# Performance work log

Measured on AMD Instinct MI355X. Metric: run time of the kernel, lower is better.

The kernel has to match this reference:

```python
import jax, jax.numpy as jnp
import numpy as np

B, OBS, H, A, E = 131072, 194, 64, 5, 3  # batch, obs dim, hidden, max_action_dim, n event types


def setup_inputs() -> dict:
    key = jax.random.key(0)
    ks = jax.random.split(key, 16)
    s = lambda k, shape, std=0.1: (jax.random.normal(k, shape, dtype=jnp.float32) * std)
    return {
        "x": jax.random.normal(ks[0], (B, OBS), dtype=jnp.float32),
        "action": jax.random.randint(ks[1], (B,), 0, A),
        "W1": s(ks[2], (OBS, H)), "b1": jnp.zeros((H,), jnp.float32),
        "W2": s(ks[3], (H, H)),   "b2": jnp.zeros((H,), jnp.float32),
        "Wh": s(ks[4], (E, H, A), 0.01), "bh": jnp.zeros((E, A), jnp.float32),
        "Wc1": s(ks[5], (OBS, H)), "bc1": jnp.zeros((H,), jnp.float32),
        "Wc2": s(ks[6], (H, H)),   "bc2": jnp.zeros((H,), jnp.float32),
        "Wc3": s(ks[7], (H, 1)),   "bc3": jnp.zeros((1,), jnp.float32),
    }


def reference(x, action, W1, b1, W2, b2, Wh, bh, Wc1, bc1, Wc2, bc2, Wc3, bc3):
    # shared trunk
    feat = jnp.tanh(jnp.tanh(x @ W1 + b1) @ W2 + b2)          # [B, H]
    # route each sample to one of E heads via argmax of first 3 obs dims
    ev = jnp.argmax(x[:, :E], axis=1)                          # [B] int
    all_logits = jnp.einsum('bh,eha->bea', feat, Wh) + bh      # [B, E, A]
    logits = jnp.take_along_axis(
        all_logits, jnp.broadcast_to(ev[:, None, None], (x.shape[0], 1, A)), axis=1
    )[:, 0]                                                    # [B, A]
    logp_all = jax.nn.log_softmax(logits, axis=-1)             # [B, A]
    logp = jnp.take_along_axis(logp_all, action[:, None], axis=1)[:, 0]  # [B]
    entropy = -jnp.sum(jnp.exp(logp_all) * logp_all, axis=-1)  # [B]
    # critic
    value = jnp.tanh(jnp.tanh(x @ Wc1 + bc1) @ Wc2 + bc2) @ Wc3 + bc3    # [B, 1]
    return action, logp, entropy, value
```

## Files before the change

### kernel.cpp

```cpp
#include <hip/hip_runtime.h>
#include <hip/hip_bf16.h>

constexpr int Bt    = 131072;
constexpr int OBS   = 194;
constexpr int NT    = 512;
constexpr int ITERS = 4;
constexpr int RS    = 72;
constexpr int LS    = 18;

constexpr int ROLE_S = 23552;

constexpr int L_W1f = 0;
constexpr int L_W2f = 28672;
constexpr int L_WHf = 45056;
constexpr int L_H   = 47104;
constexpr int L_AUX = 65536;
constexpr int L_TOT = 70144;

typedef short bf8   __attribute__((ext_vector_type(8)));
typedef float f32x4 __attribute__((ext_vector_type(4)));
typedef unsigned int u32;

__device__ __forceinline__ short f2bs(float f) {
    union { __hip_bfloat16 h; short s; } u;
    u.h = __float2bfloat16(f);
    return u.s;
}
__device__ __forceinline__ float bs2f(short s) {
    union { short s; __hip_bfloat16 h; } u;
    u.s = s;
    return __bfloat162float(u.h);
}
__device__ __forceinline__ u32 pk2(float a, float b) {
    union { __hip_bfloat162 h; u32 u; } r;
    r.h = __float22bfloat162_rn(float2{a, b});
    return r.u;
}
__device__ __forceinline__ float fast_tanh(float v) {
    v = fminf(fmaxf(v, -15.f), 15.f);
    float e = __expf(2.f * v);
    return (e - 1.f) * __builtin_amdgcn_rcpf(e + 1.f);
}
__device__ __forceinline__ void dma16(const void* g, void* s) {
    __builtin_amdgcn_global_load_lds(
        (const __attribute__((address_space(1))) u32*)g,
        (__attribute__((address_space(3))) u32*)s, 16, 0, 0);
}

__global__ void __launch_bounds__(256) prep(
    const float* __restrict__ W1, const float* __restrict__ b1,
    const float* __restrict__ W2, const float* __restrict__ Wh,
    const float* __restrict__ Wc1, const float* __restrict__ bc1,
    const float* __restrict__ Wc2, const float* __restrict__ Wc3,
    short* __restrict__ ws)
{
    const int gid = blockIdx.x * 256 + threadIdx.x;
    const int gsz = gridDim.x * 256;

    for (int i = gid; i < 14336; i += gsz) {
        int j = i & 7, l = (i >> 3) & 63, nt = (i >> 9) & 3, kb = i >> 11;
        int k = kb * 32 + ((l >> 4) << 3) + j;
        int n = nt * 16 + (l & 15);
        short v1 = 0, v2 = 0;
        if (k < OBS) {
            v1 = f2bs(W1[k * 64 + n]);
            v2 = f2bs(Wc1[k * 64 + n]);
        } else if (k == OBS) {
            v1 = f2bs(b1[n]);
            v2 = f2bs(bc1[n]);
        }
        ws[i]          = v1;
        ws[ROLE_S + i] = v2;
    }
    for (int i = gid; i < 8192; i += gsz) {
        int j = i & 7, l = (i >> 3) & 63, nt = (i >> 9) & 3, kb = i >> 11;
        int s = kb * 32 + ((l >> 4) << 3) + j;
        int kp = (s & 3) * 16 + (s >> 2);
        int n = nt * 16 + (l & 15);
        ws[14336 + i]          = f2bs(W2[kp * 64 + n]);
        ws[ROLE_S + 14336 + i] = f2bs(Wc2[kp * 64 + n]);
    }
    for (int i = gid; i < 1024; i += gsz) {
        int j = i & 7, l = (i >> 3) & 63, kb = i >> 9;
        int s = kb * 32 + ((l >> 4) << 3) + j;
        int kp = (s & 3) * 16 + (s >> 2);
        int cc = l & 15;
        float v;
        if (cc == 15) v = Wc3[kp];
        else { int e = cc / 5, a = cc - 5 * e; v = Wh[(e * 64 + kp) * 5 + a]; }
        short vs = f2bs(v);
        ws[22528 + i]          = vs;
        ws[ROLE_S + 22528 + i] = vs;
    }
}

__global__ void __launch_bounds__(NT, 4) fused_ac(
    const float* __restrict__ x, const int* __restrict__ act_in,
    const float* __restrict__ b2, const float* __restrict__ bc2,
    const float* __restrict__ bh, const float* __restrict__ bc3,
    const short* __restrict__ ws,
    float* __restrict__ out)
{
    __shared__ __align__(16) char smem[L_TOT];

    const int t    = threadIdx.x;
    const int w    = t >> 6;
    const int l    = t & 63;
    const int q    = l >> 4;
    const int c    = l & 15;
    const int b    = blockIdx.x;
    const int g    = b >> 4;
    const int role = (b >> 3) & 1;
    const int sub  = b & 7;
    const int base = g * 4096 + sub * 512;

    {
        const char* gsrc = ((const char*)ws) + (size_t)role * 47104;
        #pragma unroll
        for (int i = 0; i < 6; ++i) {
            int idx = i * NT + t;
            if (idx < 2944)
                dma16(gsrc + idx * 16, smem + idx * 16);
        }
    }

    const float* bL2 = role ? bc2 : b2;
    float b2v[4];
    #pragma unroll
    for (int nt = 0; nt < 4; ++nt) b2v[nt] = bL2[nt * 16 + c];
    float bhv = role ? bc3[0] : ((c < 15) ? bh[c] : 0.f);

    __syncthreads();

    const bf8* fL1 = reinterpret_cast<const bf8*>(smem + L_W1f);
    const bf8* fL2 = reinterpret_cast<const bf8*>(smem + L_W2f);
    const bf8* fWh = reinterpret_cast<const bf8*>(smem + L_WHf);
    short* hb = reinterpret_cast<short*>(smem + L_H + w * 2304);
    short* lw = reinterpret_cast<short*>(smem + L_AUX + w * 576);
    float* vb = reinterpret_cast<float*>(smem + L_AUX + w * 576);

    #pragma unroll 1
    for (int i = 0; i < ITERS; ++i) {
        const int gm = base + i * 128 + w * 16 + c;

        float2 raw[24]; float2 rt6 = float2{0.f, 0.f};
        {
            const float* xr = x + (size_t)gm * OBS;
            #pragma unroll
            for (int kb = 0; kb < 6; ++kb) {
                const float2* p = reinterpret_cast<const float2*>(xr + kb * 32 + q * 8);
                raw[kb * 4 + 0] = p[0]; raw[kb * 4 + 1] = p[1];
                raw[kb * 4 + 2] = p[2]; raw[kb * 4 + 3] = p[3];
            }
            if (q == 0) rt6 = *reinterpret_cast<const float2*>(xr + 192);
        }
        int act = 0;
        if (role == 0 && l < 16) act = act_in[gm];

        union AF { u32 u[4]; bf8 v; } af[7];
        #pragma unroll
        for (int kb = 0; kb < 6; ++kb) {
            af[kb].u[0] = pk2(raw[kb * 4 + 0].x, raw[kb * 4 + 0].y);
            af[kb].u[1] = pk2(raw[kb * 4 + 1].x, raw[kb * 4 + 1].y);
            af[kb].u[2] = pk2(raw[kb * 4 + 2].x, raw[kb * 4 + 2].y);
            af[kb].u[3] = pk2(raw[kb * 4 + 3].x, raw[kb * 4 + 3].y);
        }
        af[6].u[0] = 0; af[6].u[1] = 0; af[6].u[2] = 0; af[6].u[3] = 0;
        if (q == 0) {
            af[6].u[0] = pk2(rt6.x, rt6.y);
            af[6].u[1] = pk2(1.0f, 0.0f);
        }
        int ev = 0;
        {
            float bbest = raw[0].x;
            if (raw[0].y > bbest) { bbest = raw[0].y; ev = 1; }
            if (raw[1].x > bbest) { ev = 2; }
        }

        f32x4 acc[4];
        #pragma unroll
        for (int nt = 0; nt < 4; ++nt) acc[nt] = f32x4{0.f, 0.f, 0.f, 0.f};
        #pragma unroll
        for (int kb = 0; kb < 7; ++kb) {
            bf8 a = af[kb].v;
            #pragma unroll
            for (int nt = 0; nt < 4; ++nt)
                acc[nt] = __builtin_amdgcn_mfma_f32_16x16x32_bf16(a, fL1[(kb * 4 + nt) * 64 + l], acc[nt], 0, 0, 0);
        }
        #pragma unroll
        for (int r = 0; r < 4; ++r) {
            uint2 pa;
            pa.x = pk2(fast_tanh(acc[0][r]), fast_tanh(acc[1][r]));
            pa.y = pk2(fast_tanh(acc[2][r]), fast_tanh(acc[3][r]));
            *reinterpret_cast<uint2*>(&hb[(q * 4 + r) * RS + 4 * c]) = pa;
        }

        #pragma unroll
        for (int nt = 0; nt < 4; ++nt)
            acc[nt] = f32x4{b2v[nt], b2v[nt], b2v[nt], b2v[nt]};
        #pragma unroll
        for (int kb = 0; kb < 2; ++kb) {
            bf8 xa = *reinterpret_cast<const bf8*>(&hb[c * RS + kb * 32 + q * 8]);
            #pragma unroll
            for (int nt = 0; nt < 4; ++nt)
                acc[nt] = __builtin_amdgcn_mfma_f32_16x16x32_bf16(xa, fL2[(kb * 4 + nt) * 64 + l], acc[nt], 0, 0, 0);
        }
        #pragma unroll
        for (int r = 0; r < 4; ++r) {
            uint2 pa;
            pa.x = pk2(fast_tanh(acc[0][r]), fast_tanh(acc[1][r]));
            pa.y = pk2(fast_tanh(acc[2][r]), fast_tanh(acc[3][r]));
            *reinterpret_cast<uint2*>(&hb[(q * 4 + r) * RS + 4 * c]) = pa;
        }

        {
            f32x4 hd = f32x4{bhv, bhv, bhv, bhv};
            #pragma unroll
            for (int kb = 0; kb < 2; ++kb) {
                bf8 bw = fWh[kb * 64 + l];
                bf8 fa = *reinterpret_cast<const bf8*>(&hb[c * RS + kb * 32 + q * 8]);
                hd = __builtin_amdgcn_mfma_f32_16x16x32_bf16(fa, bw, hd, 0, 0, 0);
            }
            if (role == 0) {
                #pragma unroll
                for (int r = 0; r < 4; ++r)
                    lw[(q * 4 + r) * LS + c] = f2bs(hd[r]);
            } else if (c == 15) {
                #pragma unroll
                for (int r = 0; r < 4; ++r)
                    vb[q * 4 + r] = hd[r];
            }
        }

        if (role == 0) {
            if (l < 16) {
                float lg[5];
                #pragma unroll
                for (int a = 0; a < 5; ++a)
                    lg[a] = bs2f(lw[c * LS + ev * 5 + a]);
                float mx = lg[0];
                #pragma unroll
                for (int a = 1; a < 5; ++a) mx = fmaxf(mx, lg[a]);
                float se = 0.f;
                #pragma unroll
                for (int a = 0; a < 5; ++a) se += __expf(lg[a] - mx);
                float lse = __logf(se) + mx;
                float lsel = lg[0];
                #pragma unroll
                for (int a = 1; a < 5; ++a) lsel = (act == a) ? lg[a] : lsel;
                float ent = 0.f;
                #pragma unroll
                for (int a = 0; a < 5; ++a) { float lp = lg[a] - lse; ent -= __expf(lp) * lp; }

                out[gm]          = (float)act;
                out[Bt + gm]     = lsel - lse;
                out[2 * Bt + gm] = ent;
            }
        } else {
            if (l < 16)
                out[3 * Bt + gm] = vb[c];
        }
    }
}

extern "C" void kernel_launch(void* const* d_in, const int* in_sizes, int n_in,
                              void* d_out, int out_size, void* d_ws, size_t ws_size,
                              hipStream_t stream) {
    const float* x   = (const float*)d_in[0];
    const int*   act = (const int*)  d_in[1];
    const float* W1  = (const float*)d_in[2];
    const float* b1  = (const float*)d_in[3];
    const float* W2  = (const float*)d_in[4];
    const float* b2  = (const float*)d_in[5];
    const float* Wh  = (const float*)d_in[6];
    const float* bh  = (const float*)d_in[7];
    const float* Wc1 = (const float*)d_in[8];
    const float* bc1 = (const float*)d_in[9];
    const float* Wc2 = (const float*)d_in[10];
    const float* bc2 = (const float*)d_in[11];
    const float* Wc3 = (const float*)d_in[12];
    const float* bc3 = (const float*)d_in[13];
    float* out = (float*)d_out;
    short* ws  = (short*)d_ws;

    hipLaunchKernelGGL(prep, dim3(32), dim3(256), 0, stream,
                       W1, b1, W2, Wh, Wc1, bc1, Wc2, Wc3, ws);
    hipLaunchKernelGGL(fused_ac, dim3(512), dim3(NT), 0, stream,
                       x, act, b2, bc2, bh, bc3, ws, out);
}
```

Measured before the change: 183.2 us.

## Prefetch next x tile, vectorize weight prep, simplify tanh and entropy math

The main kernel now loads the next iteration's x rows into registers before computing the current one, so global latency overlaps with MFMA work. The head weight fragments are hoisted out of the loop. tanh drops the clamp and uses 1-2/(e+1), and entropy is computed in one pass from the softmax sums. The prep kernel now has each thread build and store a 16-byte fragment, launched on fewer blocks. Prefetching raises register pressure and may cut occupancy. Without the clamp, tanh now relies on how exp and rcp behave at infinity for large inputs.

```diff
diff --git a/kernel.cpp b/kernel.cpp
--- a/kernel.cpp
+++ b/kernel.cpp
@@ -37,9 +37,8 @@
     return r.u;
 }
 __device__ __forceinline__ float fast_tanh(float v) {
-    v = fminf(fmaxf(v, -15.f), 15.f);
     float e = __expf(2.f * v);
-    return (e - 1.f) * __builtin_amdgcn_rcpf(e + 1.f);
+    return fmaf(-2.f, __builtin_amdgcn_rcpf(e + 1.f), 1.f);
 }
 __device__ __forceinline__ void dma16(const void* g, void* s) {
     __builtin_amdgcn_global_load_lds(
@@ -55,42 +54,57 @@
     short* __restrict__ ws)
 {
     const int gid = blockIdx.x * 256 + threadIdx.x;
-    const int gsz = gridDim.x * 256;
-
-    for (int i = gid; i < 14336; i += gsz) {
-        int j = i & 7, l = (i >> 3) & 63, nt = (i >> 9) & 3, kb = i >> 11;
-        int k = kb * 32 + ((l >> 4) << 3) + j;
+
+    if (gid < 1792) {
+        int fi = gid;
+        int l = fi & 63, nt = (fi >> 6) & 3, kb = fi >> 8;
         int n = nt * 16 + (l & 15);
-        short v1 = 0, v2 = 0;
-        if (k < OBS) {
-            v1 = f2bs(W1[k * 64 + n]);
-            v2 = f2bs(Wc1[k * 64 + n]);
-        } else if (k == OBS) {
-            v1 = f2bs(b1[n]);
-            v2 = f2bs(bc1[n]);
-        }
-        ws[i]          = v1;
-        ws[ROLE_S + i] = v2;
-    }
-    for (int i = gid; i < 8192; i += gsz) {
-        int j = i & 7, l = (i >> 3) & 63, nt = (i >> 9) & 3, kb = i >> 11;
-        int s = kb * 32 + ((l >> 4) << 3) + j;
-        int kp = (s & 3) * 16 + (s >> 2);
+        union { bf8 v; short s[8]; } v1, v2;
+        #pragma unroll
+        for (int j = 0; j < 8; ++j) {
+            int k = kb * 32 + ((l >> 4) << 3) + j;
+            short a = 0, bvs = 0;
+            if (k < OBS) {
+                a   = f2bs(W1[k * 64 + n]);
+                bvs = f2bs(Wc1[k * 64 + n]);
+            } else if (k == OBS) {
+                a   = f2bs(b1[n]);
+                bvs = f2bs(bc1[n]);
+            }
+            v1.s[j] = a; v2.s[j] = bvs;
+        }
+        *reinterpret_cast<bf8*>(ws + fi * 8)          = v1.v;
+        *reinterpret_cast<bf8*>(ws + ROLE_S + fi * 8) = v2.v;
+    } else if (gid < 1792 + 1024) {
+        int fi = gid - 1792;
+        int l = fi & 63, nt = (fi >> 6) & 3, kb = fi >> 8;
         int n = nt * 16 + (l & 15);
-        ws[14336 + i]          = f2bs(W2[kp * 64 + n]);
-        ws[ROLE_S + 14336 + i] = f2bs(Wc2[kp * 64 + n]);
-    }
-    for (int i = gid; i < 1024; i += gsz) {
-        int j = i & 7, l = (i >> 3) & 63, kb = i >> 9;
-        int s = kb * 32 + ((l >> 4) << 3) + j;
-        int kp = (s & 3) * 16 + (s >> 2);
+        union { bf8 v; short s[8]; } v1, v2;
+        #pragma unroll
+        for (int j = 0; j < 8; ++j) {
+            int s = kb * 32 + ((l >> 4) << 3) + j;
+            int kp = (s & 3) * 16 + (s >> 2);
+            v1.s[j] = f2bs(W2[kp * 64 + n]);
+            v2.s[j] = f2bs(Wc2[kp * 64 + n]);
+        }
+        *reinterpret_cast<bf8*>(ws + 14336 + fi * 8)          = v1.v;
+        *reinterpret_cast<bf8*>(ws + ROLE_S + 14336 + fi * 8) = v2.v;
+    } else if (gid < 1792 + 1024 + 128) {
+        int fi = gid - (1792 + 1024);
+        int l = fi & 63, kb = fi >> 6;
         int cc = l & 15;
-        float v;
-        if (cc == 15) v = Wc3[kp];
-        else { int e = cc / 5, a = cc - 5 * e; v = Wh[(e * 64 + kp) * 5 + a]; }
-        short vs = f2bs(v);
-        ws[22528 + i]          = vs;
-        ws[ROLE_S + 22528 + i] = vs;
+        union { bf8 v; short s[8]; } v1;
+        #pragma unroll
+        for (int j = 0; j < 8; ++j) {
+            int s = kb * 32 + ((l >> 4) << 3) + j;
+            int kp = (s & 3) * 16 + (s >> 2);
+            float v;
+            if (cc == 15) v = Wc3[kp];
+            else { int e = cc / 5, a = cc - 5 * e; v = Wh[(e * 64 + kp) * 5 + a]; }
+            v1.s[j] = f2bs(v);
+        }
+        *reinterpret_cast<bf8*>(ws + 22528 + fi * 8)          = v1.v;
+        *reinterpret_cast<bf8*>(ws + ROLE_S + 22528 + fi * 8) = v1.v;
     }
 }
 
@@ -130,7 +144,44 @@
     for (int nt = 0; nt < 4; ++nt) b2v[nt] = bL2[nt * 16 + c];
     float bhv = role ? bc3[0] : ((c < 15) ? bh[c] : 0.f);
 
+    float2 raw[24]; float2 rt6;
+    auto loadraw = [&](int gm2) {
+        const float* xr = x + (size_t)gm2 * OBS;
+        #pragma unroll
+        for (int kb = 0; kb < 6; ++kb) {
+            const float2* p = reinterpret_cast<const float2*>(xr + kb * 32 + q * 8);
+            raw[kb * 4 + 0] = p[0]; raw[kb * 4 + 1] = p[1];
+            raw[kb * 4 + 2] = p[2]; raw[kb * 4 + 3] = p[3];
+        }
+        rt6 = float2{0.f, 0.f};
+        if (q == 0) rt6 = *reinterpret_cast<const float2*>(xr + 192);
+    };
+    union AF { u32 u[4]; bf8 v; } af[7];
+    int ev = 0;
+    auto packaf = [&]() {
+        #pragma unroll
+        for (int kb = 0; kb < 6; ++kb) {
+            af[kb].u[0] = pk2(raw[kb * 4 + 0].x, raw[kb * 4 + 0].y);
+            af[kb].u[1] = pk2(raw[kb * 4 + 1].x, raw[kb * 4 + 1].y);
+            af[kb].u[2] = pk2(raw[kb * 4 + 2].x, raw[kb * 4 + 2].y);
+            af[kb].u[3] = pk2(raw[kb * 4 + 3].x, raw[kb * 4 + 3].y);
+        }
+        af[6].u[0] = 0; af[6].u[1] = 0; af[6].u[2] = 0; af[6].u[3] = 0;
+        if (q == 0) {
+            af[6].u[0] = pk2(rt6.x, rt6.y);
+            af[6].u[1] = pk2(1.0f, 0.0f);
+        }
+        ev = 0;
+        float bbest = raw[0].x;
+        if (raw[0].y > bbest) { bbest = raw[0].y; ev = 1; }
+        if (raw[1].x > bbest) { ev = 2; }
+    };
+
+    loadraw(base + w * 16 + c);
+
     __syncthreads();
+
+    packaf();
 
     const bf8* fL1 = reinterpret_cast<const bf8*>(smem + L_W1f);
     const bf8* fL2 = reinterpret_cast<const bf8*>(smem + L_W2f);
@@ -139,43 +190,17 @@
     short* lw = reinterpret_cast<short*>(smem + L_AUX + w * 576);
     float* vb = reinterpret_cast<float*>(smem + L_AUX + w * 576);
 
+    bf8 bwh0 = fWh[l];
+    bf8 bwh1 = fWh[64 + l];
+
     #pragma unroll 1
     for (int i = 0; i < ITERS; ++i) {
         const int gm = base + i * 128 + w * 16 + c;
-
-        float2 raw[24]; float2 rt6 = float2{0.f, 0.f};
-        {
-            const float* xr = x + (size_t)gm * OBS;
-            #pragma unroll
-            for (int kb = 0; kb < 6; ++kb) {
-                const float2* p = reinterpret_cast<const float2*>(xr + kb * 32 + q * 8);
-                raw[kb * 4 + 0] = p[0]; raw[kb * 4 + 1] = p[1];
-                raw[kb * 4 + 2] = p[2]; raw[kb * 4 + 3] = p[3];
-            }
-            if (q == 0) rt6 = *reinterpret_cast<const float2*>(xr + 192);
-        }
+        const int evc = ev;
+
         int act = 0;
         if (role == 0 && l < 16) act = act_in[gm];
-
-        union AF { u32 u[4]; bf8 v; } af[7];
-        #pragma unroll
-        for (int kb = 0; kb < 6; ++kb) {
-            af[kb].u[0] = pk2(raw[kb * 4 + 0].x, raw[kb * 4 + 0].y);
-            af[kb].u[1] = pk2(raw[kb * 4 + 1].x, raw[kb * 4 + 1].y);
-            af[kb].u[2] = pk2(raw[kb * 4 + 2].x, raw[kb * 4 + 2].y);
-            af[kb].u[3] = pk2(raw[kb * 4 + 3].x, raw[kb * 4 + 3].y);
-        }
-        af[6].u[0] = 0; af[6].u[1] = 0; af[6].u[2] = 0; af[6].u[3] = 0;
-        if (q == 0) {
-            af[6].u[0] = pk2(rt6.x, rt6.y);
-            af[6].u[1] = pk2(1.0f, 0.0f);
-        }
-        int ev = 0;
-        {
-            float bbest = raw[0].x;
-            if (raw[0].y > bbest) { bbest = raw[0].y; ev = 1; }
-            if (raw[1].x > bbest) { ev = 2; }
-        }
+        if (i + 1 < ITERS) loadraw(base + (i + 1) * 128 + w * 16 + c);
 
         f32x4 acc[4];
         #pragma unroll
@@ -215,12 +240,10 @@
 
         {
             f32x4 hd = f32x4{bhv, bhv, bhv, bhv};
-            #pragma unroll
-            for (int kb = 0; kb < 2; ++kb) {
-                bf8 bw = fWh[kb * 64 + l];
-                bf8 fa = *reinterpret_cast<const bf8*>(&hb[c * RS + kb * 32 + q * 8]);
-                hd = __builtin_amdgcn_mfma_f32_16x16x32_bf16(fa, bw, hd, 0, 0, 0);
-            }
+            bf8 fa0 = *reinterpret_cast<const bf8*>(&hb[c * RS + q * 8]);
+            bf8 fa1 = *reinterpret_cast<const bf8*>(&hb[c * RS + 32 + q * 8]);
+            hd = __builtin_amdgcn_mfma_f32_16x16x32_bf16(fa0, bwh0, hd, 0, 0, 0);
+            hd = __builtin_amdgcn_mfma_f32_16x16x32_bf16(fa1, bwh1, hd, 0, 0, 0);
             if (role == 0) {
                 #pragma unroll
                 for (int r = 0; r < 4; ++r)
@@ -237,29 +260,34 @@
                 float lg[5];
                 #pragma unroll
                 for (int a = 0; a < 5; ++a)
-                    lg[a] = bs2f(lw[c * LS + ev * 5 + a]);
+                    lg[a] = bs2f(lw[c * LS + evc * 5 + a]);
                 float mx = lg[0];
                 #pragma unroll
                 for (int a = 1; a < 5; ++a) mx = fmaxf(mx, lg[a]);
-                float se = 0.f;
-                #pragma unroll
-                for (int a = 0; a < 5; ++a) se += __expf(lg[a] - mx);
-                float lse = __logf(se) + mx;
+                float se = 0.f, s2 = 0.f;
+                #pragma unroll
+                for (int a = 0; a < 5; ++a) {
+                    float d = lg[a] - mx;
+                    float e = __expf(d);
+                    se += e;
+                    s2 = fmaf(e, d, s2);
+                }
+                float lnse = __logf(se);
+                float ent  = lnse - s2 * __builtin_amdgcn_rcpf(se);
                 float lsel = lg[0];
                 #pragma unroll
                 for (int a = 1; a < 5; ++a) lsel = (act == a) ? lg[a] : lsel;
-                float ent = 0.f;
-                #pragma unroll
-                for (int a = 0; a < 5; ++a) { float lp = lg[a] - lse; ent -= __expf(lp) * lp; }
 
                 out[gm]          = (float)act;
-                out[Bt + gm]     = lsel - lse;
+                out[Bt + gm]     = lsel - (lnse + mx);
                 out[2 * Bt + gm] = ent;
             }
         } else {
             if (l < 16)
                 out[3 * Bt + gm] = vb[c];
         }
+
+        if (i + 1 < ITERS) packaf();
     }
 }
 
@@ -283,7 +311,7 @@
     float* out = (float*)d_out;
     short* ws  = (short*)d_ws;
 
-    hipLaunchKernelGGL(prep, dim3(32), dim3(256), 0, stream,
+    hipLaunchKernelGGL(prep, dim3(12), dim3(256), 0, stream,
                        W1, b1, W2, Wh, Wc1, bc1, Wc2, Wc3, ws);
     hipLaunchKernelGGL(fused_ac, dim3(512), dim3(NT), 0, stream,
                        x, act, b2, bc2, bh, bc3, ws, out);
```

New measurement: 204.9 us. +11.8%, slower.
